# Performance work log

Measured on AMD Instinct MI355X. Metric: run time of the kernel, lower is better.

The kernel has to match this reference:

```python
import jax, jax.numpy as jnp
import numpy as np

B, N, E, D, NS, H = 32, 4096, 256, 256, 8, 256
N_ITERS, N_SH, N_MESH, MESH_LR = 3, 5, 4, 5.0

def layer_norm(x, scale, bias, eps=1e-5):
    m = jnp.mean(x, axis=-1, keepdims=True)
    v = jnp.var(x, axis=-1, keepdims=True)
    return (x - m) / jnp.sqrt(v + eps) * scale + bias

def sinkhorn(C, a, b, u=None, v=None, n_iters=N_SH):
    # log-domain Sinkhorn with marginals a [B,N], b [B,S]; C [B,N,S]
    log_a, log_b = jnp.log(a), jnp.log(b)
    if u is None:
        u = jnp.zeros_like(a)
    if v is None:
        v = jnp.zeros_like(b)
    K = -C
    for _ in range(n_iters):
        u = log_a - jax.nn.logsumexp(K + v[:, None, :], axis=-1)
        v = log_b - jax.nn.logsumexp(K + u[:, :, None], axis=-2)
    attn = jnp.exp(K + u[:, :, None] + v[:, None, :])
    return attn, u, v

def minimize_entropy_of_sinkhorn(C0, a, b, mesh_lr=MESH_LR, n_mesh=N_MESH):
    # MESH: gradient-descend the cost matrix to minimize entropy of the transport plan
    def ent(C):
        attn, _, _ = sinkhorn(C, a, b)
        return -jnp.sum(attn * jnp.log(attn + 1e-8))
    C = C0
    for _ in range(n_mesh):
        C = C - mesh_lr * jax.grad(ent)(C)
    _, u, v = sinkhorn(C, a, b)
    return C, u, v

def gru_cell(x, h, Wih, Whh, bih, bhh):
    # torch.nn.GRUCell math, gate order (r, z, n)
    gi = x @ Wih.T + bih
    gh = h @ Whh.T + bhh
    ir, iz, inn = jnp.split(gi, 3, axis=-1)
    hr, hz, hn = jnp.split(gh, 3, axis=-1)
    r = jax.nn.sigmoid(ir + hr)
    z = jax.nn.sigmoid(iz + hz)
    n = jnp.tanh(inn + r * hn)
    return (1.0 - z) * n + z * h

def setup_inputs():
    key = jax.random.key(0)
    ks = jax.random.split(key, 16)
    s = 0.02
    return {
        "inputs": jax.random.normal(ks[0], (B, N, E), jnp.float32),
        "slots_init": jax.random.normal(ks[1], (B, NS, D), jnp.float32),
        "ln_in_s": jnp.ones((E,), jnp.float32), "ln_in_b": jnp.zeros((E,), jnp.float32),
        "ln_sl_s": jnp.ones((D,), jnp.float32), "ln_sl_b": jnp.zeros((D,), jnp.float32),
        "ln_mlp_s": jnp.ones((D,), jnp.float32), "ln_mlp_b": jnp.zeros((D,), jnp.float32),
        "Wq": jax.random.normal(ks[2], (D, D), jnp.float32) * s,
        "Wk": jax.random.normal(ks[3], (E, D), jnp.float32) * s,
        "Wv": jax.random.normal(ks[4], (E, D), jnp.float32) * s,
        "wi_W": jax.random.normal(ks[5], (E, 1), jnp.float32) * s, "wi_b": jnp.zeros((1,), jnp.float32),
        "ws_W": jax.random.normal(ks[6], (D, 1), jnp.float32) * s, "ws_b": jnp.zeros((1,), jnp.float32),
        "gru_Wih": jax.random.normal(ks[7], (3 * D, D), jnp.float32) * s,
        "gru_Whh": jax.random.normal(ks[8], (3 * D, D), jnp.float32) * s,
        "gru_bih": jnp.zeros((3 * D,), jnp.float32), "gru_bhh": jnp.zeros((3 * D,), jnp.float32),
        "mlp_W1": jax.random.normal(ks[9], (D, H), jnp.float32) * s, "mlp_b1": jnp.zeros((H,), jnp.float32),
        "mlp_W2": jax.random.normal(ks[10], (H, D), jnp.float32) * s, "mlp_b2": jnp.zeros((D,), jnp.float32),
    }

def reference(inputs, slots_init, ln_in_s, ln_in_b, ln_sl_s, ln_sl_b, ln_mlp_s, ln_mlp_b, Wq, Wk, Wv, wi_W, wi_b, ws_W, ws_b, gru_Wih, gru_Whh, gru_bih, gru_bhh, mlp_W1, mlp_b1, mlp_W2, mlp_b2):
    x = layer_norm(inputs, ln_in_s, ln_in_b)
    k = x @ Wk          # [B,N,D]
    v = x @ Wv          # [B,N,D]
    a = jax.nn.softmax(jnp.squeeze(x @ wi_W, -1) + wi_b[0], axis=-1) * NS  # input marginal [B,N]
    k_sq = jnp.sum(k * k, axis=-1)  # [B,N]

    def step(slots):
        sn = layer_norm(slots, ln_sl_s, ln_sl_b)
        b = jax.nn.softmax(jnp.squeeze(sn @ ws_W, -1) + ws_b[0], axis=-1) * NS  # slot marginal [B,S]
        q = sn @ Wq  # [B,S,D]
        # Euclidean cdist(k, q) via the Gram-matrix identity
        d2 = k_sq[:, :, None] + jnp.sum(q * q, -1)[:, None, :] - 2.0 * jnp.einsum('bnd,bsd->bns', k, q)
        C = jnp.sqrt(jnp.clip(d2, 1e-12))
        C, p, qpot = minimize_entropy_of_sinkhorn(C, a, b)
        attn, _, _ = sinkhorn(C, a, b, u=p, v=qpot)  # warm-started final sinkhorn
        updates = jnp.einsum('bns,bnd->bsd', attn, v)
        h = gru_cell(updates.reshape(-1, D), slots.reshape(-1, D), gru_Wih, gru_Whh, gru_bih, gru_bhh).reshape(B, NS, D)
        hn = layer_norm(h, ln_mlp_s, ln_mlp_b)
        h = h + (jax.nn.relu(hn @ mlp_W1 + mlp_b1) @ mlp_W2 + mlp_b2)
        return h, attn

    slots = slots_init
    attn = None
    for _ in range(N_ITERS - 1):
        slots, attn = step(slots)
    slots = jax.lax.stop_gradient(slots)  # .detach() before final step
    slots, attn = step(slots)
    return slots, jnp.transpose(attn, (0, 2, 1)), slots
```

## Files before the change

kernel.cpp:

```cpp
#include <hip/hip_runtime.h>
#include <hip/hip_bf16.h>

#define B_ 32
#define N_ 4096
#define E_ 256
#define D_ 256
#define NS_ 8
#define LN8 2.0794415416798357f
#define OFF_ATTN 65536
#define OFF_S2   (65536 + 1048576)
#define NSPLIT 8
#define SENT 0xFFFFFFFFu

typedef unsigned short u16;
typedef unsigned short u16x8 __attribute__((ext_vector_type(8)));
typedef __bf16 bf16x8 __attribute__((ext_vector_type(8)));
typedef float floatx4 __attribute__((ext_vector_type(4)));

__device__ __forceinline__ float bf2f(u16 h) {
  unsigned int u = ((unsigned int)h) << 16;
  return __uint_as_float(u);
}
__device__ __forceinline__ u16 f2bf(float f) {
  unsigned int u = __float_as_uint(f);
  unsigned int r = (u + 0x7FFFu + ((u >> 16) & 1u)) >> 16;
  return (u16)r;
}
__device__ __forceinline__ float ldx(const void* p, int i, int dt) {
  return dt ? ((const float*)p)[i] : bf2f(((const u16*)p)[i]);
}
__device__ __forceinline__ void stx(void* p, size_t i, int dt, float v) {
  if (dt) ((float*)p)[i] = v; else ((u16*)p)[i] = f2bf(v);
}
__device__ __forceinline__ float slog(float x) { return __logf(fmaxf(x, 1e-35f)); }
__device__ __forceinline__ float cl(float x) { return fminf(fmaxf(x, -1e30f), 1e30f); }

__device__ __forceinline__ float breduce256(float v, float* red4, int tid) {
  #pragma unroll
  for (int m = 1; m < 64; m <<= 1) v += __shfl_xor(v, m, 64);
  __syncthreads();
  if ((tid & 63) == 0) red4[tid >> 6] = v;
  __syncthreads();
  return red4[0] + red4[1] + red4[2] + red4[3];
}

__global__ void detect_dtype_kernel(const u16* __restrict__ inp, int* __restrict__ flag) {
  int lane = threadIdx.x & 63;
  int good = 0;
  for (int i = lane; i < 256; i += 64) {
    float x = bf2f(inp[i]);
    float ax = fabsf(x);
    if (x == 0.0f || (ax >= 1e-3f && ax <= 64.0f)) good++;
  }
  #pragma unroll
  for (int m = 1; m < 64; m <<= 1) good += __shfl_xor(good, m, 64);
  if (lane == 0) *flag = (good >= 208) ? 0 : 1;
}


__global__ void tr_kv_kernel(const void* __restrict__ Wk, const void* __restrict__ Wv,
                             u16* __restrict__ WkvT, const int* __restrict__ dtf) {
  const int dt = *dtf;
  int idx = blockIdx.x * 256 + threadIdx.x;
  int half = idx >> 16, i = idx & 65535;
  int r = i >> 8, c = i & 255;
  const void* src = half ? Wv : Wk;
  WkvT[((size_t)(half * 256 + c)) * 256 + r] = f2bf(ldx(src, i, dt));
}

__global__ void tr_gru_kernel(const void* __restrict__ Wih, const void* __restrict__ Whh,
                              u16* __restrict__ WihT, u16* __restrict__ WhhT,
                              const int* __restrict__ dtf) {
  const int dt = *dtf;
  int idx = blockIdx.x * 256 + threadIdx.x;
  int half = idx >= 196608;
  int i = idx - (half ? 196608 : 0);
  int r = i >> 8, c = i & 255;
  u16* dst = half ? WhhT : WihT;
  dst[(size_t)c * 768 + r] = f2bf(ldx(half ? Whh : Wih, i, dt));
}

__global__ void cast_slots_kernel(const void* __restrict__ src, float* __restrict__ dst,
                                  const int* __restrict__ dtf) {
  const int dt = *dtf;
  int i = blockIdx.x * 256 + threadIdx.x;
  dst[i] = ldx(src, i, dt);
}

__global__ __launch_bounds__(256) void ln_stats_kernel(
    const void* __restrict__ inp, const void* __restrict__ lns, const void* __restrict__ lnb,
    const void* __restrict__ wiW, const int* __restrict__ dtf,
    u16* __restrict__ xln, float* __restrict__ logits) {
  const int dt = *dtf;
  int row = blockIdx.x * 4 + (threadIdx.x >> 6);
  int lane = threadIdx.x & 63;
  float xs[4];
  if (dt) {
    float4 h = *(const float4*)((const float*)inp + (size_t)row * E_ + lane * 4);
    xs[0] = h.x; xs[1] = h.y; xs[2] = h.z; xs[3] = h.w;
  } else {
    ushort4 h = *(const ushort4*)((const u16*)inp + (size_t)row * E_ + lane * 4);
    xs[0] = bf2f(h.x); xs[1] = bf2f(h.y); xs[2] = bf2f(h.z); xs[3] = bf2f(h.w);
  }
  float s = xs[0] + xs[1] + xs[2] + xs[3];
  float q = xs[0]*xs[0] + xs[1]*xs[1] + xs[2]*xs[2] + xs[3]*xs[3];
  #pragma unroll
  for (int m = 1; m < 64; m <<= 1) { s += __shfl_xor(s, m, 64); q += __shfl_xor(q, m, 64); }
  float mean = s * (1.0f / E_);
  float var = q * (1.0f / E_) - mean * mean;
  float rstd = rsqrtf(fmaxf(var, 0.0f) + 1e-5f);
  int e = lane * 4;
  float d = 0.0f;
  float xn[4];
  #pragma unroll
  for (int j = 0; j < 4; ++j) {
    xn[j] = (xs[j] - mean) * rstd * ldx(lns, e + j, dt) + ldx(lnb, e + j, dt);
    d += xn[j] * ldx(wiW, e + j, dt);
  }
  ushort4 o;
  o.x = f2bf(xn[0]); o.y = f2bf(xn[1]); o.z = f2bf(xn[2]); o.w = f2bf(xn[3]);
  *(ushort4*)(xln + (size_t)row * E_ + e) = o;
  #pragma unroll
  for (int m = 1; m < 64; m <<= 1) d += __shfl_xor(d, m, 64);
  if (lane == 0) logits[row] = d;
}

__global__ __launch_bounds__(1024) void amarg_kernel(const float* __restrict__ logits,
    float* __restrict__ log_a, float* __restrict__ inva) {
  __shared__ float red[16];
  __shared__ float bcast;
  int b = blockIdx.x, tid = threadIdx.x;
  logits += (size_t)b * N_;
  float l[4];
  #pragma unroll
  for (int i = 0; i < 4; ++i) l[i] = logits[tid + i * 1024];
  float mx = fmaxf(fmaxf(l[0], l[1]), fmaxf(l[2], l[3]));
  #pragma unroll
  for (int m = 1; m < 64; m <<= 1) mx = fmaxf(mx, __shfl_xor(mx, m, 64));
  __syncthreads();
  if ((tid & 63) == 0) red[tid >> 6] = mx;
  __syncthreads();
  if (tid == 0) { float v = red[0]; for (int i = 1; i < 16; ++i) v = fmaxf(v, red[i]); bcast = v; }
  __syncthreads();
  float M = bcast;
  float se = 0.0f;
  #pragma unroll
  for (int i = 0; i < 4; ++i) se += __expf(l[i] - M);
  #pragma unroll
  for (int m = 1; m < 64; m <<= 1) se += __shfl_xor(se, m, 64);
  __syncthreads();
  if ((tid & 63) == 0) red[tid >> 6] = se;
  __syncthreads();
  if (tid == 0) { float v = 0; for (int i = 0; i < 16; ++i) v += red[i]; bcast = v; }
  __syncthreads();
  float lgS = slog(bcast);
  #pragma unroll
  for (int i = 0; i < 4; ++i) {
    float lav = l[i] - M - lgS + LN8;
    log_a[tid + i * 1024] = lav;
    inva[tid + i * 1024] = fminf(__expf(-lav), 1e20f);
  }
}

__global__ __launch_bounds__(256, 2) void gemm_bt_kernel(
    const u16* __restrict__ A, const u16* __restrict__ BT,
    u16* __restrict__ kbf, u16* __restrict__ vbf) {
  __shared__ __align__(16) u16 Als[128 * 32];
  __shared__ __align__(16) u16 Bls[128 * 32];
  int tid = threadIdx.x;
  int m0 = blockIdx.x * 128, n0 = blockIdx.y * 128;
  u16* ob = (n0 < 256) ? kbf : vbf;
  int nb = n0 & 255;
  int w = tid >> 6, lane = tid & 63;
  int wm = (w & 1) * 64, wn = (w >> 1) * 64;
  int fr = lane & 15, kg = lane >> 4;
  floatx4 acc[4][4];
  #pragma unroll
  for (int i = 0; i < 4; ++i)
    #pragma unroll
    for (int j = 0; j < 4; ++j) acc[i][j] = (floatx4){0.f, 0.f, 0.f, 0.f};
  int sm = tid >> 1;
  int sk0 = (tid & 1) * 16;
  const u16* arow = A + (size_t)(m0 + sm) * E_;
  const u16* brow = BT + (size_t)(n0 + sm) * E_;
  for (int kc = 0; kc < E_; kc += 32) {
    #pragma unroll
    for (int j = 0; j < 16; j += 8) {
      int kk = kc + sk0 + j;
      *(u16x8*)&Als[sm * 32 + sk0 + j] = *(const u16x8*)(arow + kk);
      *(u16x8*)&Bls[sm * 32 + sk0 + j] = *(const u16x8*)(brow + kk);
    }
    __syncthreads();
    bf16x8 af[4], bfv[4];
    #pragma unroll
    for (int im = 0; im < 4; ++im) af[im] = *(const bf16x8*)&Als[(wm + im * 16 + fr) * 32 + kg * 8];
    #pragma unroll
    for (int in = 0; in < 4; ++in) bfv[in] = *(const bf16x8*)&Bls[(wn + in * 16 + fr) * 32 + kg * 8];
    #pragma unroll
    for (int im = 0; im < 4; ++im)
      #pragma unroll
      for (int in = 0; in < 4; ++in)
        acc[im][in] = __builtin_amdgcn_mfma_f32_16x16x32_bf16(af[im], bfv[in], acc[im][in], 0, 0, 0);
    __syncthreads();
  }
  #pragma unroll
  for (int im = 0; im < 4; ++im)
    #pragma unroll
    for (int in = 0; in < 4; ++in)
      #pragma unroll
      for (int r = 0; r < 4; ++r) {
        int row = m0 + wm + im * 16 + kg * 4 + r;
        int col = nb + wn + in * 16 + fr;
        ob[(size_t)row * D_ + col] = f2bf(acc[im][in][r]);
      }
}


__global__ __launch_bounds__(256) void s1_kernel(
    const float* __restrict__ slots, const void* __restrict__ lnss, const void* __restrict__ lnsb,
    const void* __restrict__ Wq, const void* __restrict__ wsW, const int* __restrict__ dtf,
    float* __restrict__ qf, float* __restrict__ q_sq, float* __restrict__ logits_b) {
  __shared__ float sn_sh[256];
  __shared__ float red4[4];
  const int dt = *dtf;
  int row = blockIdx.x;
  int tid = threadIdx.x;
  float h = slots[(size_t)row * D_ + tid];
  float sum = breduce256(h, red4, tid);
  float sq = breduce256(h * h, red4, tid);
  float mean = sum * (1.0f / D_), var = sq * (1.0f / D_) - mean * mean;
  float rstd = rsqrtf(fmaxf(var, 0.0f) + 1e-5f);
  float sn = (h - mean) * rstd * ldx(lnss, tid, dt) + ldx(lnsb, tid, dt);
  sn_sh[tid] = sn;
  __syncthreads();
  float acc = 0.0f;
  if (dt) {
    const float* W = (const float*)Wq;
    for (int d = 0; d < 256; ++d) acc += sn_sh[d] * W[d * 256 + tid];
  } else {
    const u16* W = (const u16*)Wq;
    for (int d = 0; d < 256; ++d) acc += sn_sh[d] * bf2f(W[d * 256 + tid]);
  }
  qf[(size_t)row * 256 + tid] = acc;
  float qs = breduce256(acc * acc, red4, tid);
  float lbp = breduce256(sn * ldx(wsW, tid, dt), red4, tid);
  if (tid == 0) { q_sq[row] = qs; logits_b[row] = lbp; }
}

__device__ __forceinline__ float grp_sync_reduce(
    float acc8[8], float (*red)[8],
    unsigned int* gp, int rp, int blkn, int wv, int lane, int tid) {
  #pragma unroll
  for (int m = 1; m < 64; m <<= 1)
    #pragma unroll
    for (int s = 0; s < 8; ++s) acc8[s] += __shfl_xor(acc8[s], m, 64);
  if (lane == 0)
    #pragma unroll
    for (int s = 0; s < 8; ++s) red[wv][s] = acc8[s];
  __syncthreads();
  float x = 0.0f;
  if (tid < 64) {
    float v = red[tid >> 3][tid & 7];
    v += __shfl_xor(v, 8, 64);
    v += __shfl_xor(v, 16, 64);
    v += __shfl_xor(v, 32, 64);
    if (tid < 8)
      __hip_atomic_store(gp + rp * 64 + blkn * 8 + tid, __float_as_uint(v),
                         __ATOMIC_RELAXED, __HIP_MEMORY_SCOPE_AGENT);
    unsigned int u;
    for (;;) {
      u = __hip_atomic_load(gp + rp * 64 + tid, __ATOMIC_RELAXED, __HIP_MEMORY_SCOPE_AGENT);
      if (__all(u != SENT)) break;
      __builtin_amdgcn_s_sleep(1);
    }
    x = __uint_as_float(u);
    x += __shfl_xor(x, 8, 64);
    x += __shfl_xor(x, 16, 64);
    x += __shfl_xor(x, 32, 64);
  }
  return x;
}

__global__ __launch_bounds__(512, 2) void mesh_kernel(
    const u16* __restrict__ kbf, const u16* __restrict__ vbf,
    const float* __restrict__ qf32, const float* __restrict__ qsq_g,
    const float* __restrict__ log_a_g, const float* __restrict__ inva_g,
    const float* __restrict__ logits_b_g, const void* __restrict__ wsb,
    const int* __restrict__ dtf,
    unsigned int* __restrict__ gpart,
    float* __restrict__ updp, void* __restrict__ dout_or_null) {
  const int blkn = blockIdx.x;
  const int b = blockIdx.y;
  const int tid = threadIdx.x;
  const int dt = *dtf;
  const int n = blkn * 512 + tid;

  __shared__ float evP[6][8];
  __shared__ float lb[8], invb[8];
  __shared__ float dv[8];
  __shared__ float red[8][8];
  __shared__ float q_lds[8][256];
  __shared__ float qsq_l[8];
  __shared__ float pv_lds[512][8];

  const float la = log_a_g[(size_t)b * N_ + n];
  const float ia = inva_g[(size_t)b * N_ + n];
  unsigned int* gp = gpart + (size_t)b * 64 * 64;

  {
    const float* qb = qf32 + (size_t)b * 8 * 256;
    #pragma unroll
    for (int i = tid; i < 2048; i += 512) q_lds[i >> 8][i & 255] = qb[i];
    if (tid < 8) {
      qsq_l[tid] = qsq_g[b * 8 + tid];
      float off = ldx(wsb, 0, dt);
      float l[8], M = -1e30f;
      #pragma unroll
      for (int s = 0; s < 8; ++s) { l[s] = logits_b_g[b * 8 + s] + off; M = fmaxf(M, l[s]); }
      float S = 0.0f;
      #pragma unroll
      for (int s = 0; s < 8; ++s) S += __expf(l[s] - M);
      float lgS = slog(S);
      float x = l[tid] - M - lgS + LN8;
      lb[tid] = x; invb[tid] = fminf(__expf(-x), 1e20f);
    }
  }
  __syncthreads();

  float E[8], dK[8], eus[5];
  float eu = 0.0f, dup = 0.0f;
  {
    const u16* kp = kbf + ((size_t)b * N_ + n) * D_;
    float accq[8] = {0, 0, 0, 0, 0, 0, 0, 0};
    float kq = 0.0f;
    for (int kc = 0; kc < 256; kc += 8) {
      u16x8 kv = *(const u16x8*)(kp + kc);
      float kf[8];
      #pragma unroll
      for (int j = 0; j < 8; ++j) { kf[j] = bf2f(kv[j]); kq += kf[j] * kf[j]; }
      #pragma unroll
      for (int s = 0; s < 8; ++s) {
        float4 qa = *(const float4*)&q_lds[s][kc];
        float4 qb2 = *(const float4*)&q_lds[s][kc + 4];
        accq[s] += kf[0] * qa.x + kf[1] * qa.y + kf[2] * qa.z + kf[3] * qa.w
                 + kf[4] * qb2.x + kf[5] * qb2.y + kf[6] * qb2.z + kf[7] * qb2.w;
      }
    }
    #pragma unroll
    for (int s = 0; s < 8; ++s) {
      float d2 = kq + qsq_l[s] - 2.0f * accq[s];
      float Cv = sqrtf(fmaxf(d2, 1e-12f));
      E[s] = __expf(-Cv);
    }
  }

  const int wv = tid >> 6, lane = tid & 63;
  int rp = 0;

  for (int mesh = 0; mesh < 4; ++mesh) {
    if (tid < 8) evP[0][tid] = 1.0f;
    __syncthreads();
    for (int t = 1; t <= 5; ++t) {
      float evp[8];
      #pragma unroll
      for (int s = 0; s < 8; ++s) evp[s] = evP[t - 1][s];
      float su = 0.0f;
      #pragma unroll
      for (int s = 0; s < 8; ++s) su += fminf(E[s] * evp[s], 1e30f);
      float u = la - slog(su);
      eu = fminf(__expf(u), 1e20f);
      eus[t - 1] = eu;
      float acc8[8];
      #pragma unroll
      for (int s = 0; s < 8; ++s) acc8[s] = fminf(E[s] * eu, 1e30f);
      float S = grp_sync_reduce(acc8, red, gp, rp, blkn, wv, lane, tid);
      if (tid < 8) {
        float v = lb[tid] - slog(S);
        evP[t][tid] = fminf(__expf(v), 1e20f);
      }
      ++rp;
      __syncthreads();
    }
    {
      float ev5[8];
      #pragma unroll
      for (int s = 0; s < 8; ++s) ev5[s] = evP[5][s];
      float acc8[8];
      dup = 0.0f;
      #pragma unroll
      for (int s = 0; s < 8; ++s) {
        float t1 = fminf(E[s] * eu, 1e30f);
        float P = fminf(t1 * ev5[s], 1e30f);
        float Pe = P + 1e-8f;
        float g = -(__logf(Pe) + P / Pe) * P;
        dK[s] = g; dup += g; acc8[s] = g;
      }
      float S = grp_sync_reduce(acc8, red, gp, rp, blkn, wv, lane, tid);
      if (tid < 8) dv[tid] = cl(S);
      ++rp;
      __syncthreads();
    }
    for (int t = 5; t >= 1; --t) {
      float evt[8], evtm[8], dvl[8], ibl[8];
      #pragma unroll
      for (int s = 0; s < 8; ++s) { evt[s] = evP[t][s]; evtm[s] = evP[t - 1][s]; dvl[s] = dv[s]; ibl[s] = invb[s]; }
      float eut = eus[t - 1];
      float duv = 0.0f;
      float w8[8];
      #pragma unroll
      for (int s = 0; s < 8; ++s) {
        float a1 = fminf(E[s] * eut, 1e30f);
        float b1 = fminf(a1 * evt[s], 1e30f);
        w8[s] = fminf(b1 * ibl[s], 1e30f);
        duv += cl(dvl[s] * w8[s]);
      }
      float du = ((t == 5) ? dup : 0.0f) - duv;
      float duf = cl(cl(du * ia) * eut);
      float acc8[8];
      #pragma unroll
      for (int s = 0; s < 8; ++s) {
        float ee = fminf(E[s] * evtm[s], 1e30f);
        float zc = cl(ee * duf);
        dK[s] -= cl(dvl[s] * w8[s]) + zc;
        acc8[s] = -zc;
      }
      if (t > 1) {
        float S = grp_sync_reduce(acc8, red, gp, rp, blkn, wv, lane, tid);
        if (tid < 8) dv[tid] = cl(S);
        ++rp;
      }
      __syncthreads();
    }
    #pragma unroll
    for (int s = 0; s < 8; ++s) {
      float dkc = fminf(fmaxf(dK[s], -4.0f), 4.0f);
      float Enew = E[s] * __expf(-5.0f * dkc);
      E[s] = fminf(fmaxf(Enew, 1e-35f), 1e30f);
    }
  }

  if (tid < 8) evP[0][tid] = 1.0f;
  __syncthreads();
  for (int t = 1; t <= 10; ++t) {
    int pc = (t - 1) & 1, cc = t & 1;
    float evp[8];
    #pragma unroll
    for (int s = 0; s < 8; ++s) evp[s] = evP[pc][s];
    float su = 0.0f;
    #pragma unroll
    for (int s = 0; s < 8; ++s) su += fminf(E[s] * evp[s], 1e30f);
    eu = fminf(__expf(la - slog(su)), 1e20f);
    float acc8[8];
    #pragma unroll
    for (int s = 0; s < 8; ++s) acc8[s] = fminf(E[s] * eu, 1e30f);
    float S = grp_sync_reduce(acc8, red, gp, rp, blkn, wv, lane, tid);
    if (tid < 8) {
      float v = lb[tid] - slog(S);
      evP[cc][tid] = fminf(__expf(v), 1e20f);
    }
    ++rp;
    __syncthreads();
  }
  float evf[8];
  #pragma unroll
  for (int s = 0; s < 8; ++s) evf[s] = evP[0][s];
  float pv[8];
  #pragma unroll
  for (int s = 0; s < 8; ++s) {
    float t1 = fminf(E[s] * eu, 1e30f);
    pv[s] = fminf(t1 * evf[s], 1e30f);
  }
  if (dout_or_null) {
    #pragma unroll
    for (int s = 0; s < 8; ++s)
      stx(dout_or_null, (size_t)OFF_ATTN + ((size_t)b * 8 + s) * N_ + n, dt, pv[s]);
  }

  #pragma unroll
  for (int s = 0; s < 8; ++s) pv_lds[tid][s] = pv[s];
  __syncthreads();
  {
    int d = tid & 255, half = tid >> 8;
    const u16* vp = vbf + ((size_t)b * N_ + blkn * 512 + half * 256) * D_ + d;
    float acc[8] = {0, 0, 0, 0, 0, 0, 0, 0};
    for (int i = 0; i < 256; ++i) {
      float vv = bf2f(vp[(size_t)i * D_]);
      float4 a0 = *(const float4*)&pv_lds[half * 256 + i][0];
      float4 a1 = *(const float4*)&pv_lds[half * 256 + i][4];
      acc[0] += a0.x * vv; acc[1] += a0.y * vv; acc[2] += a0.z * vv; acc[3] += a0.w * vv;
      acc[4] += a1.x * vv; acc[5] += a1.y * vv; acc[6] += a1.z * vv; acc[7] += a1.w * vv;
    }
    __syncthreads();
    if (half == 1) {
      #pragma unroll
      for (int s = 0; s < 8; ++s) pv_lds[d][s] = acc[s];
    }
    __syncthreads();
    if (half == 0) {
      #pragma unroll
      for (int s = 0; s < 8; ++s) acc[s] += pv_lds[d][s];
      #pragma unroll
      for (int s = 0; s < 8; ++s)
        updp[(((size_t)b * 8 + blkn) * 8 + s) * D_ + d] = acc[s];
    }
  }
}

__global__ __launch_bounds__(256) void gru_s1_kernel(
    const float* __restrict__ updp, const float* __restrict__ slots_cur,
    const u16* __restrict__ WihT, const u16* __restrict__ WhhT,
    const void* __restrict__ bih, const void* __restrict__ bhh,
    const void* __restrict__ lnms, const void* __restrict__ lnmb,
    const void* __restrict__ W1, const void* __restrict__ b1,
    const void* __restrict__ W2, const void* __restrict__ b2,
    const void* __restrict__ lnss, const void* __restrict__ lnsb,
    const void* __restrict__ Wq, const void* __restrict__ wsW,
    const int* __restrict__ dtf, int do_s1,
    float* __restrict__ slots_next, float* __restrict__ qf,
    float* __restrict__ q_sq, float* __restrict__ logits_b,
    void* __restrict__ dout_or_null) {
  __shared__ float xs[256], hs[256], hns[256], as_[256];
  __shared__ float red4[4];
  const int dt = *dtf;
  int row = blockIdx.x;
  int b = row >> 3, s = row & 7;
  int tid = threadIdx.x;
  float x = 0.0f;
  #pragma unroll
  for (int c = 0; c < 8; ++c) x += updp[(((size_t)b * 8 + c) * 8 + s) * D_ + tid];
  float h = slots_cur[(size_t)row * D_ + tid];
  xs[tid] = x; hs[tid] = h;
  __syncthreads();
  float gr = ldx(bih, tid, dt), gz = ldx(bih, 256 + tid, dt), gn = ldx(bih, 512 + tid, dt);
  float hr = ldx(bhh, tid, dt), hz = ldx(bhh, 256 + tid, dt), hn_ = ldx(bhh, 512 + tid, dt);
  for (int e = 0; e < 256; ++e) {
    float xe = xs[e], he = hs[e];
    const u16* wi = WihT + e * 768;
    const u16* wh = WhhT + e * 768;
    gr += xe * bf2f(wi[tid]); gz += xe * bf2f(wi[256 + tid]); gn += xe * bf2f(wi[512 + tid]);
    hr += he * bf2f(wh[tid]); hz += he * bf2f(wh[256 + tid]); hn_ += he * bf2f(wh[512 + tid]);
  }
  float r = 1.0f / (1.0f + __expf(-(gr + hr)));
  float z = 1.0f / (1.0f + __expf(-(gz + hz)));
  float nn = tanhf(gn + r * hn_);
  float h2 = (1.0f - z) * nn + z * h;
  float sum = breduce256(h2, red4, tid);
  float sq = breduce256(h2 * h2, red4, tid);
  float mean = sum * (1.0f / D_), var = sq * (1.0f / D_) - mean * mean;
  float rstd = rsqrtf(fmaxf(var, 0.0f) + 1e-5f);
  float hn2 = (h2 - mean) * rstd * ldx(lnms, tid, dt) + ldx(lnmb, tid, dt);
  hns[tid] = hn2;
  __syncthreads();
  float a1 = ldx(b1, tid, dt);
  if (dt) {
    const float* W = (const float*)W1;
    for (int e = 0; e < 256; ++e) a1 += hns[e] * W[e * 256 + tid];
  } else {
    const u16* W = (const u16*)W1;
    for (int e = 0; e < 256; ++e) a1 += hns[e] * bf2f(W[e * 256 + tid]);
  }
  a1 = fmaxf(a1, 0.0f);
  as_[tid] = a1;
  __syncthreads();
  float o = h2 + ldx(b2, tid, dt);
  if (dt) {
    const float* W = (const float*)W2;
    for (int e = 0; e < 256; ++e) o += as_[e] * W[e * 256 + tid];
  } else {
    const u16* W = (const u16*)W2;
    for (int e = 0; e < 256; ++e) o += as_[e] * bf2f(W[e * 256 + tid]);
  }
  slots_next[(size_t)row * D_ + tid] = o;
  if (dout_or_null) {
    stx(dout_or_null, (size_t)row * D_ + tid, dt, o);
    stx(dout_or_null, (size_t)OFF_S2 + (size_t)row * D_ + tid, dt, o);
  }
  if (do_s1) {
    float sum2 = breduce256(o, red4, tid);
    float sq2 = breduce256(o * o, red4, tid);
    float mean2 = sum2 * (1.0f / D_), var2 = sq2 * (1.0f / D_) - mean2 * mean2;
    float rstd2 = rsqrtf(fmaxf(var2, 0.0f) + 1e-5f);
    float sn = (o - mean2) * rstd2 * ldx(lnss, tid, dt) + ldx(lnsb, tid, dt);
    __syncthreads();
    xs[tid] = sn;
    __syncthreads();
    float accq = 0.0f;
    if (dt) {
      const float* W = (const float*)Wq;
      for (int d = 0; d < 256; ++d) accq += xs[d] * W[d * 256 + tid];
    } else {
      const u16* W = (const u16*)Wq;
      for (int d = 0; d < 256; ++d) accq += xs[d] * bf2f(W[d * 256 + tid]);
    }
    qf[(size_t)row * 256 + tid] = accq;
    float qs = breduce256(accq * accq, red4, tid);
    float lbp = breduce256(sn * ldx(wsW, tid, dt), red4, tid);
    if (tid == 0) { q_sq[row] = qs; logits_b[row] = lbp; }
  }
}


extern "C" void kernel_launch(void* const* d_in, const int* in_sizes, int n_in,
                              void* d_out, int out_size, void* d_ws, size_t ws_size,
                              hipStream_t stream) {
  (void)in_sizes; (void)n_in; (void)out_size;
  const void* inp      = d_in[0];
  const void* slots0   = d_in[1];
  const void* ln_in_s  = d_in[2];
  const void* ln_in_b  = d_in[3];
  const void* ln_sl_s  = d_in[4];
  const void* ln_sl_b  = d_in[5];
  const void* ln_mlp_s = d_in[6];
  const void* ln_mlp_b = d_in[7];
  const void* Wq  = d_in[8];
  const void* Wk  = d_in[9];
  const void* Wv  = d_in[10];
  const void* wiW = d_in[11];
  const void* wsW = d_in[13];
  const void* wsb = d_in[14];
  const void* Wih = d_in[15];
  const void* Whh = d_in[16];
  const void* bih = d_in[17];
  const void* bhh = d_in[18];
  const void* W1  = d_in[19];
  const void* b1  = d_in[20];
  const void* W2  = d_in[21];
  const void* b2  = d_in[22];

  char* ws = (char*)d_ws;
  size_t off = 0;
  auto alloc = [&](size_t bytes) -> void* {
    void* p = ws + off;
    off += (bytes + 255) & ~(size_t)255;
    return p;
  };
  const size_t NR = (size_t)B_ * N_;
  int* dtflag     = (int*)alloc(256);
  float* logits_a = (float*)alloc(NR * 4);
  float* log_a    = (float*)alloc(NR * 4);
  float* inva     = (float*)alloc(NR * 4);
  u16* xln        = (u16*)alloc(NR * E_ * 2);
  u16* kbf        = (u16*)alloc(NR * D_ * 2);
  u16* vbf        = (u16*)alloc(NR * D_ * 2);
  u16* WkvT       = (u16*)alloc((size_t)512 * 256 * 2);
  u16* WihT       = (u16*)alloc(768 * 256 * 2);
  u16* WhhT       = (u16*)alloc(768 * 256 * 2);
  float* qf32     = (float*)alloc((size_t)B_ * 8 * 256 * 4);
  float* q_sq     = (float*)alloc(B_ * 8 * 4);
  float* logits_b = (float*)alloc(B_ * 8 * 4);
  float* updp     = (float*)alloc((size_t)B_ * 8 * 8 * D_ * 4);
  float* slots_a  = (float*)alloc((size_t)B_ * 8 * D_ * 4);
  float* slots_b  = (float*)alloc((size_t)B_ * 8 * D_ * 4);
  unsigned int* gpart = (unsigned int*)alloc((size_t)3 * B_ * 64 * 64 * 4);
  if (ws_size < off) return;

  hipMemsetAsync(gpart, 0xFF, (size_t)3 * B_ * 64 * 64 * 4, stream);
  detect_dtype_kernel<<<1, 64, 0, stream>>>((const u16*)inp, dtflag);

  tr_kv_kernel<<<512, 256, 0, stream>>>(Wk, Wv, WkvT, dtflag);
  tr_gru_kernel<<<1536, 256, 0, stream>>>(Wih, Whh, WihT, WhhT, dtflag);
  cast_slots_kernel<<<(B_ * 8 * D_) / 256, 256, 0, stream>>>(slots0, slots_a, dtflag);
  ln_stats_kernel<<<NR / 4, 256, 0, stream>>>(inp, ln_in_s, ln_in_b, wiW, dtflag, xln, logits_a);
  amarg_kernel<<<B_, 1024, 0, stream>>>(logits_a, log_a, inva);
  gemm_bt_kernel<<<dim3(NR / 128, 4), 256, 0, stream>>>(xln, WkvT, kbf, vbf);

  float* scur = slots_a;
  float* snext = slots_b;
  s1_kernel<<<B_ * 8, 256, 0, stream>>>(scur, ln_sl_s, ln_sl_b, Wq, wsW, dtflag, qf32, q_sq, logits_b);
  for (int step = 0; step < 3; ++step) {
    bool last = (step == 2);
    mesh_kernel<<<dim3(NSPLIT, B_), 512, 0, stream>>>(kbf, vbf, qf32, q_sq, log_a, inva,
                                                      logits_b, wsb, dtflag,
                                                      gpart + (size_t)step * B_ * 64 * 64,
                                                      updp, last ? d_out : (void*)nullptr);
    gru_s1_kernel<<<B_ * 8, 256, 0, stream>>>(updp, scur, WihT, WhhT, bih, bhh,
                                              ln_mlp_s, ln_mlp_b, W1, b1, W2, b2,
                                              ln_sl_s, ln_sl_b, Wq, wsW, dtflag, last ? 0 : 1,
                                              snext, qf32, q_sq, logits_b,
                                              last ? d_out : (void*)nullptr);
    float* t = scur; scur = snext; snext = t;
  }
}
```

Before: 1.000 ms.

## Parallelize GRU gate matvecs across 768 threads with row-major vector loads

The GRU kernel now launches 768 threads per slot row, one per gate output, instead of 256 threads each computing three gates. The GRU weights are cast to bf16 in their original row-major layout rather than transposed, so each thread reads its own weight row with 8-wide vector loads. Gate results go through shared memory before the nonlinearity, and the later MLP and Q stages stay on 256 threads with the other 512 idle. This is meant to cut the serial length of the GRU matvec loop, at the cost of per-thread strided row reads that do not coalesce across lanes and extra barriers.

```diff
diff --git a/kernel.cpp b/kernel.cpp
--- a/kernel.cpp
+++ b/kernel.cpp
@@ -44,6 +44,15 @@
   return red4[0] + red4[1] + red4[2] + red4[3];
 }
 
+__device__ __forceinline__ float breduce768(float v, float* red4, int tid) {
+  #pragma unroll
+  for (int m = 1; m < 64; m <<= 1) v += __shfl_xor(v, m, 64);
+  __syncthreads();
+  if (tid < 256 && (tid & 63) == 0) red4[tid >> 6] = v;
+  __syncthreads();
+  return red4[0] + red4[1] + red4[2] + red4[3];
+}
+
 __global__ void detect_dtype_kernel(const u16* __restrict__ inp, int* __restrict__ flag) {
   int lane = threadIdx.x & 63;
   int good = 0;
@@ -68,16 +77,15 @@
   WkvT[((size_t)(half * 256 + c)) * 256 + r] = f2bf(ldx(src, i, dt));
 }
 
-__global__ void tr_gru_kernel(const void* __restrict__ Wih, const void* __restrict__ Whh,
-                              u16* __restrict__ WihT, u16* __restrict__ WhhT,
+__global__ void cast_w_kernel(const void* __restrict__ Wih, const void* __restrict__ Whh,
+                              u16* __restrict__ WihB, u16* __restrict__ WhhB,
                               const int* __restrict__ dtf) {
   const int dt = *dtf;
   int idx = blockIdx.x * 256 + threadIdx.x;
   int half = idx >= 196608;
   int i = idx - (half ? 196608 : 0);
-  int r = i >> 8, c = i & 255;
-  u16* dst = half ? WhhT : WihT;
-  dst[(size_t)c * 768 + r] = f2bf(ldx(half ? Whh : Wih, i, dt));
+  u16* dst = half ? WhhB : WihB;
+  dst[i] = f2bf(ldx(half ? Whh : Wih, i, dt));
 }
 
 __global__ void cast_slots_kernel(const void* __restrict__ src, float* __restrict__ dst,
@@ -506,9 +514,9 @@
   }
 }
 
-__global__ __launch_bounds__(256) void gru_s1_kernel(
+__global__ __launch_bounds__(768) void gru_s1_kernel(
     const float* __restrict__ updp, const float* __restrict__ slots_cur,
-    const u16* __restrict__ WihT, const u16* __restrict__ WhhT,
+    const u16* __restrict__ WihB, const u16* __restrict__ WhhB,
     const void* __restrict__ bih, const void* __restrict__ bhh,
     const void* __restrict__ lnms, const void* __restrict__ lnmb,
     const void* __restrict__ W1, const void* __restrict__ b1,
@@ -520,81 +528,105 @@
     float* __restrict__ q_sq, float* __restrict__ logits_b,
     void* __restrict__ dout_or_null) {
   __shared__ float xs[256], hs[256], hns[256], as_[256];
+  __shared__ float gi_sh[768], gh_sh[768];
   __shared__ float red4[4];
   const int dt = *dtf;
   int row = blockIdx.x;
   int b = row >> 3, s = row & 7;
   int tid = threadIdx.x;
-  float x = 0.0f;
-  #pragma unroll
-  for (int c = 0; c < 8; ++c) x += updp[(((size_t)b * 8 + c) * 8 + s) * D_ + tid];
-  float h = slots_cur[(size_t)row * D_ + tid];
-  xs[tid] = x; hs[tid] = h;
-  __syncthreads();
-  float gr = ldx(bih, tid, dt), gz = ldx(bih, 256 + tid, dt), gn = ldx(bih, 512 + tid, dt);
-  float hr = ldx(bhh, tid, dt), hz = ldx(bhh, 256 + tid, dt), hn_ = ldx(bhh, 512 + tid, dt);
-  for (int e = 0; e < 256; ++e) {
-    float xe = xs[e], he = hs[e];
-    const u16* wi = WihT + e * 768;
-    const u16* wh = WhhT + e * 768;
-    gr += xe * bf2f(wi[tid]); gz += xe * bf2f(wi[256 + tid]); gn += xe * bf2f(wi[512 + tid]);
-    hr += he * bf2f(wh[tid]); hz += he * bf2f(wh[256 + tid]); hn_ += he * bf2f(wh[512 + tid]);
-  }
-  float r = 1.0f / (1.0f + __expf(-(gr + hr)));
-  float z = 1.0f / (1.0f + __expf(-(gz + hz)));
-  float nn = tanhf(gn + r * hn_);
-  float h2 = (1.0f - z) * nn + z * h;
-  float sum = breduce256(h2, red4, tid);
-  float sq = breduce256(h2 * h2, red4, tid);
+  if (tid < 256) {
+    float x = 0.0f;
+    #pragma unroll
+    for (int c = 0; c < 8; ++c) x += updp[(((size_t)b * 8 + c) * 8 + s) * D_ + tid];
+    xs[tid] = x;
+    hs[tid] = slots_cur[(size_t)row * D_ + tid];
+  }
+  __syncthreads();
+  {
+    float gi = ldx(bih, tid, dt);
+    float gh = ldx(bhh, tid, dt);
+    const u16* wi = WihB + (size_t)tid * 256;
+    const u16* wh = WhhB + (size_t)tid * 256;
+    for (int e = 0; e < 256; e += 8) {
+      u16x8 a = *(const u16x8*)(wi + e);
+      u16x8 c = *(const u16x8*)(wh + e);
+      #pragma unroll
+      for (int j = 0; j < 8; ++j) gi += xs[e + j] * bf2f(a[j]);
+      #pragma unroll
+      for (int j = 0; j < 8; ++j) gh += hs[e + j] * bf2f(c[j]);
+    }
+    gi_sh[tid] = gi; gh_sh[tid] = gh;
+  }
+  __syncthreads();
+  float h2 = 0.0f;
+  if (tid < 256) {
+    float r = 1.0f / (1.0f + __expf(-(gi_sh[tid] + gh_sh[tid])));
+    float z = 1.0f / (1.0f + __expf(-(gi_sh[256 + tid] + gh_sh[256 + tid])));
+    float nn = tanhf(gi_sh[512 + tid] + r * gh_sh[512 + tid]);
+    h2 = (1.0f - z) * nn + z * hs[tid];
+  }
+  float sum = breduce768(h2, red4, tid);
+  float sq = breduce768(h2 * h2, red4, tid);
   float mean = sum * (1.0f / D_), var = sq * (1.0f / D_) - mean * mean;
   float rstd = rsqrtf(fmaxf(var, 0.0f) + 1e-5f);
-  float hn2 = (h2 - mean) * rstd * ldx(lnms, tid, dt) + ldx(lnmb, tid, dt);
-  hns[tid] = hn2;
-  __syncthreads();
-  float a1 = ldx(b1, tid, dt);
-  if (dt) {
-    const float* W = (const float*)W1;
-    for (int e = 0; e < 256; ++e) a1 += hns[e] * W[e * 256 + tid];
-  } else {
-    const u16* W = (const u16*)W1;
-    for (int e = 0; e < 256; ++e) a1 += hns[e] * bf2f(W[e * 256 + tid]);
-  }
-  a1 = fmaxf(a1, 0.0f);
-  as_[tid] = a1;
-  __syncthreads();
-  float o = h2 + ldx(b2, tid, dt);
-  if (dt) {
-    const float* W = (const float*)W2;
-    for (int e = 0; e < 256; ++e) o += as_[e] * W[e * 256 + tid];
-  } else {
-    const u16* W = (const u16*)W2;
-    for (int e = 0; e < 256; ++e) o += as_[e] * bf2f(W[e * 256 + tid]);
-  }
-  slots_next[(size_t)row * D_ + tid] = o;
-  if (dout_or_null) {
-    stx(dout_or_null, (size_t)row * D_ + tid, dt, o);
-    stx(dout_or_null, (size_t)OFF_S2 + (size_t)row * D_ + tid, dt, o);
+  if (tid < 256) {
+    float hn2 = (h2 - mean) * rstd * ldx(lnms, tid, dt) + ldx(lnmb, tid, dt);
+    hns[tid] = hn2;
+  }
+  __syncthreads();
+  float o = 0.0f;
+  if (tid < 256) {
+    float a1 = ldx(b1, tid, dt);
+    if (dt) {
+      const float* W = (const float*)W1;
+      for (int e = 0; e < 256; ++e) a1 += hns[e] * W[e * 256 + tid];
+    } else {
+      const u16* W = (const u16*)W1;
+      for (int e = 0; e < 256; ++e) a1 += hns[e] * bf2f(W[e * 256 + tid]);
+    }
+    as_[tid] = fmaxf(a1, 0.0f);
+  }
+  __syncthreads();
+  if (tid < 256) {
+    o = h2 + ldx(b2, tid, dt);
+    if (dt) {
+      const float* W = (const float*)W2;
+      for (int e = 0; e < 256; ++e) o += as_[e] * W[e * 256 + tid];
+    } else {
+      const u16* W = (const u16*)W2;
+      for (int e = 0; e < 256; ++e) o += as_[e] * bf2f(W[e * 256 + tid]);
+    }
+    slots_next[(size_t)row * D_ + tid] = o;
+    if (dout_or_null) {
+      stx(dout_or_null, (size_t)row * D_ + tid, dt, o);
+      stx(dout_or_null, (size_t)OFF_S2 + (size_t)row * D_ + tid, dt, o);
+    }
   }
   if (do_s1) {
-    float sum2 = breduce256(o, red4, tid);
-    float sq2 = breduce256(o * o, red4, tid);
+    float sum2 = breduce768(o, red4, tid);
+    float sq2 = breduce768(o * o, red4, tid);
     float mean2 = sum2 * (1.0f / D_), var2 = sq2 * (1.0f / D_) - mean2 * mean2;
     float rstd2 = rsqrtf(fmaxf(var2, 0.0f) + 1e-5f);
-    float sn = (o - mean2) * rstd2 * ldx(lnss, tid, dt) + ldx(lnsb, tid, dt);
+    float sn = 0.0f;
     __syncthreads();
-    xs[tid] = sn;
+    if (tid < 256) {
+      sn = (o - mean2) * rstd2 * ldx(lnss, tid, dt) + ldx(lnsb, tid, dt);
+      xs[tid] = sn;
+    }
     __syncthreads();
     float accq = 0.0f;
-    if (dt) {
-      const float* W = (const float*)Wq;
-      for (int d = 0; d < 256; ++d) accq += xs[d] * W[d * 256 + tid];
-    } else {
-      const u16* W = (const u16*)Wq;
-      for (int d = 0; d < 256; ++d) accq += xs[d] * bf2f(W[d * 256 + tid]);
-    }
-    qf[(size_t)row * 256 + tid] = accq;
-    float qs = breduce256(accq * accq, red4, tid);
-    float lbp = breduce256(sn * ldx(wsW, tid, dt), red4, tid);
+    if (tid < 256) {
+      if (dt) {
+        const float* W = (const float*)Wq;
+        for (int d = 0; d < 256; ++d) accq += xs[d] * W[d * 256 + tid];
+      } else {
+        const u16* W = (const u16*)Wq;
+        for (int d = 0; d < 256; ++d) accq += xs[d] * bf2f(W[d * 256 + tid]);
+      }
+      qf[(size_t)row * 256 + tid] = accq;
+    }
+    float qs = breduce768(accq * accq, red4, tid);
+    float lbp = breduce768(tid < 256 ? sn * ldx(wsW, tid, dt) : 0.0f, red4, tid);
     if (tid == 0) { q_sq[row] = qs; logits_b[row] = lbp; }
   }
 }
@@ -643,8 +675,8 @@
   u16* kbf        = (u16*)alloc(NR * D_ * 2);
   u16* vbf        = (u16*)alloc(NR * D_ * 2);
   u16* WkvT       = (u16*)alloc((size_t)512 * 256 * 2);
-  u16* WihT       = (u16*)alloc(768 * 256 * 2);
-  u16* WhhT       = (u16*)alloc(768 * 256 * 2);
+  u16* WihB       = (u16*)alloc(768 * 256 * 2);
+  u16* WhhB       = (u16*)alloc(768 * 256 * 2);
   float* qf32     = (float*)alloc((size_t)B_ * 8 * 256 * 4);
   float* q_sq     = (float*)alloc(B_ * 8 * 4);
   float* logits_b = (float*)alloc(B_ * 8 * 4);
@@ -658,7 +690,7 @@
   detect_dtype_kernel<<<1, 64, 0, stream>>>((const u16*)inp, dtflag);
 
   tr_kv_kernel<<<512, 256, 0, stream>>>(Wk, Wv, WkvT, dtflag);
-  tr_gru_kernel<<<1536, 256, 0, stream>>>(Wih, Whh, WihT, WhhT, dtflag);
+  cast_w_kernel<<<1536, 256, 0, stream>>>(Wih, Whh, WihB, WhhB, dtflag);
   cast_slots_kernel<<<(B_ * 8 * D_) / 256, 256, 0, stream>>>(slots0, slots_a, dtflag);
   ln_stats_kernel<<<NR / 4, 256, 0, stream>>>(inp, ln_in_s, ln_in_b, wiW, dtflag, xln, logits_a);
   amarg_kernel<<<B_, 1024, 0, stream>>>(logits_a, log_a, inva);
@@ -673,7 +705,7 @@
                                                       logits_b, wsb, dtflag,
                                                       gpart + (size_t)step * B_ * 64 * 64,
                                                       updp, last ? d_out : (void*)nullptr);
-    gru_s1_kernel<<<B_ * 8, 256, 0, stream>>>(updp, scur, WihT, WhhT, bih, bhh,
+    gru_s1_kernel<<<B_ * 8, 768, 0, stream>>>(updp, scur, WihB, WhhB, bih, bhh,
                                               ln_mlp_s, ln_mlp_b, W1, b1, W2, b2,
                                               ln_sl_s, ln_sl_b, Wq, wsW, dtflag, last ? 0 : 1,
                                               snext, qf32, q_sq, logits_b,
```

New measurement: 993.2 us. Within noise of the previous version (-0.7%).
